# Performance work log

Measured on AMD Instinct MI355X. Metric: run time of the kernel, lower is better.

The kernel has to match this reference:

```python
import jax, jax.numpy as jnp
import numpy as np

B, L, D, H, NE, M, NP, C, F2 = 2, 1024, 768, 12, 42, 8, 1722, 97, 256


def setup_inputs() -> dict:
    key = jax.random.key(0)
    ks = jax.random.split(key, 12)
    s = 0.02
    sequence_output = jax.random.normal(ks[0], (B, L, D), jnp.float32)
    attention = jax.random.uniform(ks[1], (B, H, L, L), jnp.float32)
    mention_idx = jax.random.randint(ks[2], (B, NE, M), 0, L)
    mention_mask = jax.random.randint(ks[3], (B, NE, M), 0, 2).at[:, :, 0].set(1)
    hts = jax.random.randint(ks[4], (B, NP, 2), 0, NE)
    return dict(
        sequence_output=sequence_output, attention=attention,
        mention_idx=mention_idx, mention_mask=mention_mask, hts=hts,
        W_lin=jax.random.normal(ks[5], (D, 3)) * s, b_lin=jnp.zeros((3,)),
        W_seg=jax.random.normal(ks[6], (3, F2)) * s, b_seg=jnp.zeros((F2,)),
        W_head=jax.random.normal(ks[7], (D, F2)) * s, b_head=jnp.zeros((F2,)),
        W_tail=jax.random.normal(ks[8], (D, F2)) * s, b_tail=jnp.zeros((F2,)),
        W_bil=jax.random.normal(ks[9], (C, F2, F2)) * s, b_bil=jnp.zeros((C,)),
    )


def reference(sequence_output, attention, mention_idx, mention_mask, hts,
              W_lin, b_lin, W_seg, b_seg, W_head, b_head, W_tail, b_tail,
              W_bil, b_bil):
    b_, l_, d_ = sequence_output.shape
    h_ = attention.shape[1]
    ne, m_ = mention_idx.shape[1:]
    NEG = jnp.asarray(-1e30, sequence_output.dtype)
    msk = mention_mask.astype(sequence_output.dtype)  # [B,NE,M]

    bidx = jnp.arange(b_)[:, None, None]
    # --- get_hrt: per-entity mention gather + logsumexp pool / mean pool ---
    ment_emb = sequence_output[bidx, mention_idx]              # [B,NE,M,D]
    ent_emb = jax.nn.logsumexp(jnp.where(msk[..., None] > 0, ment_emb, NEG), axis=2)  # [B,NE,D]
    ment_att = attention[bidx, :, mention_idx]                 # [B,NE,M,H,L]
    ent_att = (ment_att * msk[..., None, None]).sum(2) / msk.sum(2)[..., None, None]  # [B,NE,H,L]

    b2 = jnp.arange(b_)[:, None]
    hs = ent_emb[b2, hts[..., 0]]                              # [B,NP,D]
    ts = ent_emb[b2, hts[..., 1]]

    # --- get_channel_map: all ne*ne pair attention-weighted context ---
    hi = jnp.repeat(jnp.arange(ne), ne)
    ti = jnp.tile(jnp.arange(ne), ne)
    h_att = ent_att[:, hi]                                     # [B,NE*NE,H,L]
    t_att = ent_att[:, ti]
    ht_att = jnp.einsum('bphl,bphl->bpl', h_att, t_att) / h_   # mean over heads
    ht_att = ht_att / (ht_att.sum(-1, keepdims=True) + 1e-5)
    rs = jnp.einsum('bld,bpl->bpd', sequence_output, ht_att)   # [B,NE*NE,D]
    feature_map = rs.reshape(b_, ne, ne, d_)

    # self.linear (D->3) then segmentation net (stand-in: 1x1 conv 3->F2 + relu)
    attn_input = feature_map @ W_lin + b_lin                   # [B,NE,NE,3]
    attn_map = jax.nn.relu(attn_input @ W_seg + b_seg)         # [B,NE,NE,F2]

    # --- get_ht: gather pair features ---
    h_t = attn_map[b2, hts[..., 0], hts[..., 1]]               # [B,NP,F2]
    hs = jnp.tanh(hs @ W_head + b_head + h_t)
    ts = jnp.tanh(ts @ W_tail + b_tail + h_t)
    logits = jnp.einsum('bpi,oij,bpj->bpo', hs, W_bil, ts) + b_bil
    return logits.reshape(-1, logits.shape[-1])               # [B*NP, C]
```

## Files before the change

kernel.cpp:

```cpp
#include <hip/hip_runtime.h>
#include <hip/hip_bf16.h>
#include <math.h>

constexpr int BB = 2;
constexpr int LL = 1024;
constexpr int DD = 768;
constexpr int HH = 12;
constexpr int NEz = 42;
constexpr int MM = 8;
constexpr int NPp = 1722;
constexpr int CC = 97;
constexpr int FF = 256;
constexpr int PAIRS = NEz * NEz;
constexpr int TOTAL = BB * NPp;
constexpr int MTv = 128;
constexpr int NTt = 28;
constexpr int PADR = 3584;
constexpr int NOGv = 36;
constexpr int NWGv = 1008;

typedef float f32x4 __attribute__((ext_vector_type(4)));
typedef short bf16x8 __attribute__((ext_vector_type(8)));
typedef unsigned int u32x2 __attribute__((ext_vector_type(2)));

__device__ inline short f2bs(float x) {
    __hip_bfloat16 b = __float2bfloat16(x);
    return *(short*)&b;
}
__device__ inline void gload16(const void* g, void* l) {
    __builtin_amdgcn_global_load_lds((const __attribute__((address_space(1))) unsigned int*)g,
                                     (__attribute__((address_space(3))) unsigned int*)l, 16, 0, 0);
}

__global__ void k_ent_emb(const float* __restrict__ seq, const int* __restrict__ midx,
                          const int* __restrict__ mmask, float* __restrict__ ent_emb) {
    int be = blockIdx.x;
    int b = be / NEz;
    int tid = threadIdx.x;
    int idx[MM], msk[MM];
#pragma unroll
    for (int m = 0; m < MM; ++m) {
        idx[m] = midx[be * MM + m];
        msk[m] = mmask[be * MM + m];
    }
    const float* sb = seq + (size_t)b * LL * DD;
    for (int d = tid; d < DD; d += 256) {
        float v[MM];
        float mx = -1e30f;
#pragma unroll
        for (int m = 0; m < MM; ++m) {
            v[m] = msk[m] ? sb[(size_t)idx[m] * DD + d] : -1e30f;
            mx = fmaxf(mx, v[m]);
        }
        float s = 0.f;
#pragma unroll
        for (int m = 0; m < MM; ++m) s += expf(v[m] - mx);
        ent_emb[(size_t)be * DD + d] = mx + logf(s);
    }
}

__global__ void k_ent_att(const float* __restrict__ att, const int* __restrict__ midx,
                          const int* __restrict__ mmask, float* __restrict__ ea) {
    int beh = blockIdx.x;
    int h = beh % HH;
    int be = beh / HH;
    int b = be / NEz;
    int tid = threadIdx.x;
    int idx[MM], msk[MM];
    float msum = 0.f;
#pragma unroll
    for (int m = 0; m < MM; ++m) {
        idx[m] = midx[be * MM + m];
        msk[m] = mmask[be * MM + m];
        msum += (float)msk[m];
    }
    float inv = 1.f / msum;
    const float* ab = att + ((size_t)b * HH + h) * LL * LL;
#pragma unroll
    for (int li = 0; li < 4; ++li) {
        int l = tid + li * 256;
        float acc = 0.f;
#pragma unroll
        for (int m = 0; m < MM; ++m)
            if (msk[m]) acc += ab[(size_t)idx[m] * LL + l];
        ea[(size_t)beh * LL + l] = acc * inv;
    }
}

__global__ void k_pairAB(const float* __restrict__ ea, const float* __restrict__ seq,
                         const float* __restrict__ Wl, float* __restrict__ szp) {
    int lcb = blockIdx.x;
    int b = blockIdx.y;
    int l0 = lcb * 8;
    int tid = threadIdx.x;
    int lane = tid & 63;
    int e1 = (tid >> 6) * 8 + (lane >> 3);
    int l = lane & 7;

    __shared__ float S[NEz][HH][9];
    __shared__ float sw[8][3];
    __shared__ float swp[24][17];

    for (int idx = tid; idx < NEz * HH * 8; idx += 384) {
        int e = idx / 96, rem = idx % 96;
        int h = rem / 8, ll = rem % 8;
        S[e][h][ll] = ea[((size_t)(b * NEz + e) * HH + h) * LL + l0 + ll];
    }
    {
        int cpair = tid % 24, s = tid / 24;
        if (s < 16) {
            int ll = cpair / 3, kk = cpair % 3;
            const float* sr = seq + ((size_t)b * LL + l0 + ll) * DD;
            float p = 0.f;
            for (int d = s * 48; d < s * 48 + 48; ++d) p += sr[d] * Wl[d * 3 + kk];
            swp[cpair][s] = p;
        }
    }
    __syncthreads();
    if (tid < 24) {
        float s = 0.f;
#pragma unroll
        for (int i = 0; i < 16; ++i) s += swp[tid][i];
        sw[tid / 3][tid % 3] = s;
    }
    __syncthreads();

    bool act = e1 < NEz;
    float e1r[HH];
#pragma unroll
    for (int h = 0; h < HH; ++h) e1r[h] = act ? S[e1][h][l] : 0.f;
    float sw0 = sw[l][0], sw1 = sw[l][1], sw2 = sw[l][2];

    for (int e2 = 0; e2 < NEz; ++e2) {
        float ht = 0.f;
#pragma unroll
        for (int h = 0; h < HH; ++h) ht += e1r[h] * S[e2][h][l];
        ht *= (1.0f / HH);
        float v0 = ht, v1 = ht * sw0, v2 = ht * sw1, v3 = ht * sw2;
#pragma unroll
        for (int off = 1; off < 8; off <<= 1) {
            v0 += __shfl_xor(v0, off);
            v1 += __shfl_xor(v1, off);
            v2 += __shfl_xor(v2, off);
            v3 += __shfl_xor(v3, off);
        }
        if (act && l == 0) {
            float4 o4 = make_float4(v0, v1, v2, v3);
            *(float4*)&szp[(((size_t)(b * PAIRS + e1 * NEz + e2)) * 128 + lcb) * 4] = o4;
        }
    }
}

__global__ void k_zz(const float* __restrict__ szp, const float* __restrict__ blin,
                     float* __restrict__ zz) {
    int idx = blockIdx.x * 256 + threadIdx.x;
    int bp = idx >> 3, s8 = idx & 7;
    if (bp >= BB * PAIRS) return;
    const float4* s = (const float4*)(szp + (size_t)bp * 512) + s8 * 16;
    float v0 = 0.f, v1 = 0.f, v2 = 0.f, v3 = 0.f;
#pragma unroll
    for (int i = 0; i < 16; ++i) {
        float4 a = s[i];
        v0 += a.x; v1 += a.y; v2 += a.z; v3 += a.w;
    }
#pragma unroll
    for (int off = 1; off < 8; off <<= 1) {
        v0 += __shfl_xor(v0, off);
        v1 += __shfl_xor(v1, off);
        v2 += __shfl_xor(v2, off);
        v3 += __shfl_xor(v3, off);
    }
    if (s8 == 0) {
        float inv = 1.f / (v0 + 1e-5f);
        float4 o4 = make_float4(v1 * inv + blin[0], v2 * inv + blin[1], v3 * inv + blin[2], 0.f);
        *(float4*)&zz[(size_t)bp * 4] = o4;
    }
}

__global__ void k_ew(const float* __restrict__ ent_emb, const float* __restrict__ Wh,
                     const float* __restrict__ bh, const float* __restrict__ Wt,
                     const float* __restrict__ bt, float* __restrict__ EWh,
                     float* __restrict__ EWt) {
    int be = blockIdx.x;
    int tid = threadIdx.x;
    __shared__ float e[DD];
    for (int d = tid; d < DD; d += 256) e[d] = ent_emb[(size_t)be * DD + d];
    __syncthreads();
    float ah = bh[tid], at = bt[tid];
    for (int d = 0; d < DD; ++d) {
        float ev = e[d];
        ah += ev * Wh[(size_t)d * FF + tid];
        at += ev * Wt[(size_t)d * FF + tid];
    }
    EWh[(size_t)be * FF + tid] = ah;
    EWt[(size_t)be * FF + tid] = at;
}

__global__ void k_wt(const float* __restrict__ Wb, char* __restrict__ Wf) {
    int o = blockIdx.x >> 2, kc = blockIdx.x & 3;
    int tid = threadIdx.x;
    __shared__ float t64[64][257];
    const float* src = Wb + (size_t)o * FF * FF + (size_t)(kc * 64) * FF;
#pragma unroll
    for (int i = 0; i < 64; ++i) {
        int flat = i * 256 + tid;
        t64[flat >> 8][flat & 255] = src[flat];
    }
    __syncthreads();
    char* dst = Wf + ((size_t)o * 4 + kc) * 32768;
#pragma unroll
    for (int i = 0; i < 8; ++i) {
        int u = i * 256 + tid;
        int c = u >> 3, k16 = u & 7;
        bf16x8 v;
#pragma unroll
        for (int j = 0; j < 8; ++j) v[j] = f2bs(t64[k16 * 8 + j][c]);
        *(bf16x8*)(dst + ((c * 128 + k16 * 16) ^ ((c & 7) << 4))) = v;
    }
}

__global__ void k_prep(const float* __restrict__ EWh, const float* __restrict__ EWt,
                       const float* __restrict__ zz, const float* __restrict__ Wseg,
                       const float* __restrict__ bseg, const int* __restrict__ hts,
                       char* __restrict__ HSf, unsigned short* __restrict__ TSt) {
    int tile = blockIdx.x >> 1, half = blockIdx.x & 1;
    int tid = threadIdx.x;
    int p0 = tile * MTv;

    __shared__ int offh[128];
    __shared__ float zr[128][3];
    __shared__ float wsg[4][128];
    __shared__ float Et[128][133];

    if (tid < 128) {
        int p = p0 + tid;
        if (p < TOTAL) {
            int b = p / NPp;
            int e1 = hts[p * 2], e2 = hts[p * 2 + 1];
            offh[tid] = (b * NEz + e1) * FF;
            float4 z4 = *(const float4*)(zz + (size_t)(b * PAIRS + e1 * NEz + e2) * 4);
            zr[tid][0] = z4.x; zr[tid][1] = z4.y; zr[tid][2] = z4.z;
        } else {
            offh[tid] = -1;
            zr[tid][0] = zr[tid][1] = zr[tid][2] = 0.f;
        }
        int c = half * 128 + tid;
        wsg[0][tid] = Wseg[c];
        wsg[1][tid] = Wseg[FF + c];
        wsg[2][tid] = Wseg[2 * FF + c];
        wsg[3][tid] = bseg[c];
    }
    {
        int r2 = tid >> 1, hc = tid & 1;
        int p = p0 + r2;
        int ot = -1;
        if (p < TOTAL) {
            int b = p / NPp;
            int e2 = hts[p * 2 + 1];
            ot = (b * NEz + e2) * FF;
        }
#pragma unroll
        for (int j = 0; j < 64; j += 4) {
            float4 v = make_float4(0.f, 0.f, 0.f, 0.f);
            if (ot >= 0) v = *(const float4*)(EWt + ot + half * 128 + hc * 64 + j);
            int cl = hc * 64 + j;
            Et[r2][cl] = v.x; Et[r2][cl + 1] = v.y; Et[r2][cl + 2] = v.z; Et[r2][cl + 3] = v.w;
        }
    }
    __syncthreads();

    char* dst = HSf + (size_t)tile * 65536;
#pragma unroll
    for (int i = 0; i < 8; ++i) {
        int u = i * 256 + tid;
        int r = u >> 4, k16 = u & 15;
        int oh = offh[r];
        bf16x8 v = {0, 0, 0, 0, 0, 0, 0, 0};
        if (oh >= 0) {
#pragma unroll
            for (int j = 0; j < 8; ++j) {
                int cl = k16 * 8 + j;
                float ht = fmaxf(zr[r][0] * wsg[0][cl] + zr[r][1] * wsg[1][cl] +
                                 zr[r][2] * wsg[2][cl] + wsg[3][cl], 0.f);
                v[j] = f2bs(tanhf(EWh[oh + half * 128 + cl] + ht));
            }
        }
        int byte = (r * 512 + half * 256 + k16 * 16) ^ ((r & 7) << 4);
        *(bf16x8*)(dst + byte) = v;
    }
    {
        int r = tid & 127, cg = tid >> 7;
        int p = p0 + r;
        bool act = p < TOTAL;
        for (int i2 = 0; i2 < 64; ++i2) {
            int cl = cg * 64 + i2;
            unsigned short v = 0;
            if (act) {
                float ht = fmaxf(zr[r][0] * wsg[0][cl] + zr[r][1] * wsg[1][cl] +
                                 zr[r][2] * wsg[2][cl] + wsg[3][cl], 0.f);
                v = (unsigned short)f2bs(tanhf(Et[r][cl] + ht));
            }
            TSt[(size_t)(half * 128 + cl) * PADR + p0 + r] = v;
        }
    }
}

#define STAGE(C, BUF) do { \
    int c_ = (C); \
    int o_ = og + NOGv * (c_ >> 2); \
    int kc_ = c_ & 3; \
    const char* Bs_ = Wf + ((size_t)(o_ * 4 + kc_)) * 32768; \
    _Pragma("unroll") \
    for (int i_ = 0; i_ < 4; ++i_) \
        gload16(Bs_ + (i_ * 512 + tid) * 16, Bb[BUF] + (i_ * 512 + tid) * 16); \
} while (0)

__launch_bounds__(512, 2)
__global__ void k_bil(const char* __restrict__ HSf, const unsigned short* __restrict__ TSt,
                      const char* __restrict__ Wf, const float* __restrict__ bbil,
                      float* __restrict__ out) {
    int f = blockIdx.x;
    int x = f & 7, sub = f >> 3;
    int q = x >> 1, h = x & 1;
    int og = q * 9 + sub / 14;
    int mt = h * 14 + sub % 14;
    int p0 = mt * MTv;
    int nO = (og < 25) ? 3 : 2;

    int tid = threadIdx.x;
    int lane = tid & 63, w = tid >> 6;
    int wr = w >> 2, wc = w & 3;
    int lr = lane & 15, lg = lane >> 4;

    __shared__ char A_l[65536];
    __shared__ char Bb[2][32768];
    __shared__ float red[MTv][4];

    u32x2 tsv[4][4];
#pragma unroll
    for (int mi = 0; mi < 4; ++mi)
#pragma unroll
        for (int ni = 0; ni < 4; ++ni)
            tsv[mi][ni] = *(const u32x2*)(TSt + (size_t)(wc * 64 + ni * 16 + lr) * PADR +
                                          p0 + wr * 64 + mi * 16 + lg * 4);

    {
        const char* As = HSf + (size_t)mt * 65536;
#pragma unroll
        for (int i = 0; i < 8; ++i)
            gload16(As + (i * 512 + tid) * 16, A_l + (i * 512 + tid) * 16);
    }
    STAGE(0, 0);
    STAGE(1, 1);

    f32x4 acc[4][4];
#pragma unroll
    for (int mi = 0; mi < 4; ++mi)
#pragma unroll
        for (int ni = 0; ni < 4; ++ni) acc[mi][ni] = (f32x4){0.f, 0.f, 0.f, 0.f};

    int T = 4 * nO;
    for (int t = 0; t < T; ++t) {
        int cur = t & 1;
        int kc = t & 3;
        __builtin_amdgcn_sched_barrier(0);
        asm volatile("s_waitcnt vmcnt(4)" ::: "memory");
        __builtin_amdgcn_sched_barrier(0);
        __builtin_amdgcn_s_barrier();
        __builtin_amdgcn_sched_barrier(0);

        const char* Bc = Bb[cur];
        int kA = kc * 128 + lg * 16;
        int kB = kA + 64;

        bf16x8 a0[4], b0[4];
#pragma unroll
        for (int mi = 0; mi < 4; ++mi) {
            int r = wr * 64 + mi * 16 + lr;
            a0[mi] = *(const bf16x8*)(A_l + ((r * 512 + kA) ^ ((r & 7) << 4)));
        }
#pragma unroll
        for (int ni = 0; ni < 4; ++ni) {
            int c = wc * 64 + ni * 16 + lr;
            b0[ni] = *(const bf16x8*)(Bc + ((c * 128 + lg * 16) ^ ((c & 7) << 4)));
        }
        __builtin_amdgcn_sched_barrier(0);
        asm volatile("s_waitcnt lgkmcnt(0)" ::: "memory");
        __builtin_amdgcn_sched_barrier(0);
        __builtin_amdgcn_s_setprio(1);
#pragma unroll
        for (int mi = 0; mi < 4; ++mi)
#pragma unroll
            for (int ni = 0; ni < 4; ++ni)
                acc[mi][ni] = __builtin_amdgcn_mfma_f32_16x16x32_bf16(a0[mi], b0[ni], acc[mi][ni], 0, 0, 0);
        __builtin_amdgcn_s_setprio(0);

        bf16x8 a1[4], b1[4];
#pragma unroll
        for (int mi = 0; mi < 4; ++mi) {
            int r = wr * 64 + mi * 16 + lr;
            a1[mi] = *(const bf16x8*)(A_l + ((r * 512 + kB) ^ ((r & 7) << 4)));
        }
#pragma unroll
        for (int ni = 0; ni < 4; ++ni) {
            int c = wc * 64 + ni * 16 + lr;
            b1[ni] = *(const bf16x8*)(Bc + ((c * 128 + 64 + lg * 16) ^ ((c & 7) << 4)));
        }
        __builtin_amdgcn_sched_barrier(0);
        asm volatile("s_waitcnt lgkmcnt(0)" ::: "memory");
        __builtin_amdgcn_sched_barrier(0);
        __builtin_amdgcn_s_barrier();
        __builtin_amdgcn_sched_barrier(0);

        int tt = (t + 2 < T) ? t + 2 : T - 1;
        STAGE(tt, cur);
        __builtin_amdgcn_sched_barrier(0);
        __builtin_amdgcn_s_setprio(1);
#pragma unroll
        for (int mi = 0; mi < 4; ++mi)
#pragma unroll
            for (int ni = 0; ni < 4; ++ni)
                acc[mi][ni] = __builtin_amdgcn_mfma_f32_16x16x32_bf16(a1[mi], b1[ni], acc[mi][ni], 0, 0, 0);
        __builtin_amdgcn_s_setprio(0);

        if ((t & 3) == 3) {
            int o = og + NOGv * (t >> 2);
#pragma unroll
            for (int mi = 0; mi < 4; ++mi) {
                float s0 = 0.f, s1 = 0.f, s2 = 0.f, s3 = 0.f;
#pragma unroll
                for (int ni = 0; ni < 4; ++ni) {
                    unsigned lo = tsv[mi][ni][0], hi = tsv[mi][ni][1];
                    s0 += acc[mi][ni][0] * __uint_as_float(lo << 16);
                    s1 += acc[mi][ni][1] * __uint_as_float(lo & 0xFFFF0000u);
                    s2 += acc[mi][ni][2] * __uint_as_float(hi << 16);
                    s3 += acc[mi][ni][3] * __uint_as_float(hi & 0xFFFF0000u);
                    acc[mi][ni] = (f32x4){0.f, 0.f, 0.f, 0.f};
                }
#pragma unroll
                for (int off = 1; off < 16; off <<= 1) {
                    s0 += __shfl_xor(s0, off);
                    s1 += __shfl_xor(s1, off);
                    s2 += __shfl_xor(s2, off);
                    s3 += __shfl_xor(s3, off);
                }
                if (lr == 0) {
                    int rb = wr * 64 + mi * 16 + lg * 4;
                    red[rb + 0][wc] = s0;
                    red[rb + 1][wc] = s1;
                    red[rb + 2][wc] = s2;
                    red[rb + 3][wc] = s3;
                }
            }
            __builtin_amdgcn_sched_barrier(0);
            asm volatile("s_waitcnt lgkmcnt(0)" ::: "memory");
            __builtin_amdgcn_sched_barrier(0);
            __builtin_amdgcn_s_barrier();
            __builtin_amdgcn_sched_barrier(0);
            if (tid < MTv) {
                int p = p0 + tid;
                if (p < TOTAL)
                    out[(size_t)p * CC + o] =
                        red[tid][0] + red[tid][1] + red[tid][2] + red[tid][3] + bbil[o];
            }
        }
    }
}
#undef STAGE

extern "C" void kernel_launch(void* const* d_in, const int* in_sizes, int n_in,
                              void* d_out, int out_size, void* d_ws, size_t ws_size,
                              hipStream_t stream) {
    const float* seq   = (const float*)d_in[0];
    const float* att   = (const float*)d_in[1];
    const int*   midx  = (const int*)d_in[2];
    const int*   mmask = (const int*)d_in[3];
    const int*   hts   = (const int*)d_in[4];
    const float* Wlin  = (const float*)d_in[5];
    const float* blin  = (const float*)d_in[6];
    const float* Wseg  = (const float*)d_in[7];
    const float* bseg  = (const float*)d_in[8];
    const float* Whead = (const float*)d_in[9];
    const float* bhead = (const float*)d_in[10];
    const float* Wtail = (const float*)d_in[11];
    const float* btail = (const float*)d_in[12];
    const float* Wbil  = (const float*)d_in[13];
    const float* bbil  = (const float*)d_in[14];
    float* out = (float*)d_out;

    float* ws = (float*)d_ws;
    float* ent_emb = ws;
    float* ea      = ent_emb + BB * NEz * DD;
    float* szp     = ea + (size_t)BB * NEz * HH * LL;
    float* zz      = szp + (size_t)BB * PAIRS * 128 * 4;
    float* EWh     = zz + (size_t)BB * PAIRS * 4;
    float* EWt     = EWh + BB * NEz * FF;
    char* Wf       = (char*)(EWt + BB * NEz * FF);
    char* HSf      = Wf + (size_t)CC * 4 * 32768;
    unsigned short* TSt = (unsigned short*)(HSf + (size_t)NTt * 65536);

    k_ent_emb<<<BB * NEz, 256, 0, stream>>>(seq, midx, mmask, ent_emb);
    k_ent_att<<<BB * NEz * HH, 256, 0, stream>>>(att, midx, mmask, ea);
    k_pairAB<<<dim3(128, BB), 384, 0, stream>>>(ea, seq, Wlin, szp);
    k_zz<<<(BB * PAIRS * 8 + 255) / 256, 256, 0, stream>>>(szp, blin, zz);
    k_ew<<<BB * NEz, 256, 0, stream>>>(ent_emb, Whead, bhead, Wtail, btail, EWh, EWt);
    k_wt<<<CC * 4, 256, 0, stream>>>(Wbil, Wf);
    k_prep<<<NTt * 2, 256, 0, stream>>>(EWh, EWt, zz, Wseg, bseg, hts, HSf, TSt);
    k_bil<<<NWGv, 512, 0, stream>>>(HSf, TSt, Wf, bbil, out);
}
```

Measured before the change: 199.0 us.

## Split bilinear K across workgroups with 256-row tiles and atomic accumulation

The bilinear kernel now uses 256-pair M tiles and splits the 256-wide reduction into two halves handled by different workgroups. Partial logits are combined with atomicAdd into an output zeroed by a memset, and the bias is added only by the first half. The head/tail projection kernel is split four ways along D, writing partial sums that the prep kernel adds up. The prep kernel is rebuilt to emit per-K-chunk swizzled A tiles and vectorized transposed tail stores. The aim is more reuse of each staged W_bil block and more parallelism in the small kernels, at the cost of atomics, an extra memset, and higher register pressure from the doubled accumulator tile.

```diff
diff --git a/kernel.cpp b/kernel.cpp
--- a/kernel.cpp
+++ b/kernel.cpp
@@ -13,11 +13,12 @@
 constexpr int FF = 256;
 constexpr int PAIRS = NEz * NEz;
 constexpr int TOTAL = BB * NPp;
-constexpr int MTv = 128;
-constexpr int NTt = 28;
+constexpr int MTv = 256;
+constexpr int NTt = 14;
 constexpr int PADR = 3584;
 constexpr int NOGv = 36;
 constexpr int NWGv = 1008;
+constexpr int EWSZ = BB * NEz * FF;
 
 typedef float f32x4 __attribute__((ext_vector_type(4)));
 typedef short bf16x8 __attribute__((ext_vector_type(8)));
@@ -179,21 +180,25 @@
 
 __global__ void k_ew(const float* __restrict__ ent_emb, const float* __restrict__ Wh,
                      const float* __restrict__ bh, const float* __restrict__ Wt,
-                     const float* __restrict__ bt, float* __restrict__ EWh,
-                     float* __restrict__ EWt) {
+                     const float* __restrict__ bt, float* __restrict__ EWph,
+                     float* __restrict__ EWpt) {
     int be = blockIdx.x;
-    int tid = threadIdx.x;
-    __shared__ float e[DD];
-    for (int d = tid; d < DD; d += 256) e[d] = ent_emb[(size_t)be * DD + d];
+    int dc = blockIdx.y;
+    int tid = threadIdx.x;
+    __shared__ float e[192];
+    if (tid < 192) e[tid] = ent_emb[(size_t)be * DD + dc * 192 + tid];
     __syncthreads();
-    float ah = bh[tid], at = bt[tid];
-    for (int d = 0; d < DD; ++d) {
+    float ah = (dc == 0) ? bh[tid] : 0.f;
+    float at = (dc == 0) ? bt[tid] : 0.f;
+    const float* Whb = Wh + (size_t)dc * 192 * FF;
+    const float* Wtb = Wt + (size_t)dc * 192 * FF;
+    for (int d = 0; d < 192; ++d) {
         float ev = e[d];
-        ah += ev * Wh[(size_t)d * FF + tid];
-        at += ev * Wt[(size_t)d * FF + tid];
-    }
-    EWh[(size_t)be * FF + tid] = ah;
-    EWt[(size_t)be * FF + tid] = at;
+        ah += ev * Whb[(size_t)d * FF + tid];
+        at += ev * Wtb[(size_t)d * FF + tid];
+    }
+    EWph[(size_t)dc * EWSZ + be * FF + tid] = ah;
+    EWpt[(size_t)dc * EWSZ + be * FF + tid] = at;
 }
 
 __global__ void k_wt(const float* __restrict__ Wb, char* __restrict__ Wf) {
@@ -219,96 +224,96 @@
     }
 }
 
-__global__ void k_prep(const float* __restrict__ EWh, const float* __restrict__ EWt,
+__global__ void k_prep(const float* __restrict__ EWph, const float* __restrict__ EWpt,
                        const float* __restrict__ zz, const float* __restrict__ Wseg,
                        const float* __restrict__ bseg, const int* __restrict__ hts,
                        char* __restrict__ HSf, unsigned short* __restrict__ TSt) {
-    int tile = blockIdx.x >> 1, half = blockIdx.x & 1;
-    int tid = threadIdx.x;
-    int p0 = tile * MTv;
-
-    __shared__ int offh[128];
-    __shared__ float zr[128][3];
-    __shared__ float wsg[4][128];
-    __shared__ float Et[128][133];
-
-    if (tid < 128) {
+    int mt = blockIdx.x >> 2, kc = blockIdx.x & 3;
+    int tid = threadIdx.x;
+    int p0 = mt * MTv;
+
+    __shared__ int offh[256], offt[256];
+    __shared__ float zr[256][3];
+    __shared__ float wsg[4][64];
+
+    {
         int p = p0 + tid;
         if (p < TOTAL) {
             int b = p / NPp;
             int e1 = hts[p * 2], e2 = hts[p * 2 + 1];
             offh[tid] = (b * NEz + e1) * FF;
+            offt[tid] = (b * NEz + e2) * FF;
             float4 z4 = *(const float4*)(zz + (size_t)(b * PAIRS + e1 * NEz + e2) * 4);
             zr[tid][0] = z4.x; zr[tid][1] = z4.y; zr[tid][2] = z4.z;
         } else {
-            offh[tid] = -1;
+            offh[tid] = -1; offt[tid] = -1;
             zr[tid][0] = zr[tid][1] = zr[tid][2] = 0.f;
         }
-        int c = half * 128 + tid;
-        wsg[0][tid] = Wseg[c];
-        wsg[1][tid] = Wseg[FF + c];
-        wsg[2][tid] = Wseg[2 * FF + c];
-        wsg[3][tid] = bseg[c];
-    }
-    {
-        int r2 = tid >> 1, hc = tid & 1;
-        int p = p0 + r2;
-        int ot = -1;
-        if (p < TOTAL) {
-            int b = p / NPp;
-            int e2 = hts[p * 2 + 1];
-            ot = (b * NEz + e2) * FF;
-        }
-#pragma unroll
-        for (int j = 0; j < 64; j += 4) {
-            float4 v = make_float4(0.f, 0.f, 0.f, 0.f);
-            if (ot >= 0) v = *(const float4*)(EWt + ot + half * 128 + hc * 64 + j);
-            int cl = hc * 64 + j;
-            Et[r2][cl] = v.x; Et[r2][cl + 1] = v.y; Et[r2][cl + 2] = v.z; Et[r2][cl + 3] = v.w;
+        if (tid < 64) {
+            int c = kc * 64 + tid;
+            wsg[0][tid] = Wseg[c];
+            wsg[1][tid] = Wseg[FF + c];
+            wsg[2][tid] = Wseg[2 * FF + c];
+            wsg[3][tid] = bseg[c];
         }
     }
     __syncthreads();
 
-    char* dst = HSf + (size_t)tile * 65536;
-#pragma unroll
-    for (int i = 0; i < 8; ++i) {
-        int u = i * 256 + tid;
-        int r = u >> 4, k16 = u & 15;
+    char* dst = HSf + (size_t)(mt * 4 + kc) * 32768;
+#pragma unroll
+    for (int it = 0; it < 8; ++it) {
+        int slot = it * 256 + tid;
+        int r = slot >> 3;
+        int kin = (slot & 7) * 16;
+        int kb = kin ^ ((r & 7) << 4);
+        int cl0 = kb >> 1;
         int oh = offh[r];
         bf16x8 v = {0, 0, 0, 0, 0, 0, 0, 0};
         if (oh >= 0) {
+            float z0 = zr[r][0], z1 = zr[r][1], z2 = zr[r][2];
+            int gc = oh + kc * 64 + cl0;
 #pragma unroll
             for (int j = 0; j < 8; ++j) {
-                int cl = k16 * 8 + j;
-                float ht = fmaxf(zr[r][0] * wsg[0][cl] + zr[r][1] * wsg[1][cl] +
-                                 zr[r][2] * wsg[2][cl] + wsg[3][cl], 0.f);
-                v[j] = f2bs(tanhf(EWh[oh + half * 128 + cl] + ht));
+                int cl = cl0 + j;
+                float ew = EWph[gc + j] + EWph[EWSZ + gc + j] +
+                           EWph[2 * EWSZ + gc + j] + EWph[3 * EWSZ + gc + j];
+                float ht = fmaxf(z0 * wsg[0][cl] + z1 * wsg[1][cl] +
+                                 z2 * wsg[2][cl] + wsg[3][cl], 0.f);
+                v[j] = f2bs(tanhf(ew + ht));
             }
         }
-        int byte = (r * 512 + half * 256 + k16 * 16) ^ ((r & 7) << 4);
-        *(bf16x8*)(dst + byte) = v;
+        *(bf16x8*)(dst + r * 128 + kin) = v;
     }
     {
-        int r = tid & 127, cg = tid >> 7;
-        int p = p0 + r;
-        bool act = p < TOTAL;
-        for (int i2 = 0; i2 < 64; ++i2) {
-            int cl = cg * 64 + i2;
-            unsigned short v = 0;
-            if (act) {
-                float ht = fmaxf(zr[r][0] * wsg[0][cl] + zr[r][1] * wsg[1][cl] +
-                                 zr[r][2] * wsg[2][cl] + wsg[3][cl], 0.f);
-                v = (unsigned short)f2bs(tanhf(Et[r][cl] + ht));
+        int cl = tid >> 2, rgg = tid & 3;
+        int c = kc * 64 + cl;
+        float w0 = wsg[0][cl], w1 = wsg[1][cl], w2 = wsg[2][cl], w3 = wsg[3][cl];
+#pragma unroll
+        for (int v8 = 0; v8 < 8; ++v8) {
+            int rbase = rgg * 64 + v8 * 8;
+            bf16x8 w;
+#pragma unroll
+            for (int j = 0; j < 8; ++j) {
+                int r = rbase + j;
+                int ot = offt[r];
+                short vv = 0;
+                if (ot >= 0) {
+                    float ew = EWpt[ot + c] + EWpt[EWSZ + ot + c] +
+                               EWpt[2 * EWSZ + ot + c] + EWpt[3 * EWSZ + ot + c];
+                    float ht = fmaxf(zr[r][0] * w0 + zr[r][1] * w1 + zr[r][2] * w2 + w3, 0.f);
+                    vv = f2bs(tanhf(ew + ht));
+                }
+                w[j] = vv;
             }
-            TSt[(size_t)(half * 128 + cl) * PADR + p0 + r] = v;
+            *(bf16x8*)(TSt + (size_t)c * PADR + p0 + rbase) = w;
         }
     }
 }
 
 #define STAGE(C, BUF) do { \
     int c_ = (C); \
-    int o_ = og + NOGv * (c_ >> 2); \
-    int kc_ = c_ & 3; \
+    int o_ = og + NOGv * (c_ >> 1); \
+    int kc_ = kr2 + (c_ & 1); \
     const char* Bs_ = Wf + ((size_t)(o_ * 4 + kc_)) * 32768; \
     _Pragma("unroll") \
     for (int i_ = 0; i_ < 4; ++i_) \
@@ -320,10 +325,11 @@
                       const char* __restrict__ Wf, const float* __restrict__ bbil,
                       float* __restrict__ out) {
     int f = blockIdx.x;
-    int x = f & 7, sub = f >> 3;
-    int q = x >> 1, h = x & 1;
-    int og = q * 9 + sub / 14;
-    int mt = h * 14 + sub % 14;
+    int xcd = f & 7, sub = f >> 3;
+    int q = xcd >> 1, kr = xcd & 1;
+    int og = q + 4 * (sub / 14);
+    int mt = sub % 14;
+    int kr2 = kr * 2;
     int p0 = mt * MTv;
     int nO = (og < 25) ? 3 : 2;
 
@@ -336,48 +342,49 @@
     __shared__ char Bb[2][32768];
     __shared__ float red[MTv][4];
 
-    u32x2 tsv[4][4];
-#pragma unroll
-    for (int mi = 0; mi < 4; ++mi)
+    u32x2 tsv[8][4];
+#pragma unroll
+    for (int mi = 0; mi < 8; ++mi)
 #pragma unroll
         for (int ni = 0; ni < 4; ++ni)
             tsv[mi][ni] = *(const u32x2*)(TSt + (size_t)(wc * 64 + ni * 16 + lr) * PADR +
-                                          p0 + wr * 64 + mi * 16 + lg * 4);
+                                          p0 + wr * 128 + mi * 16 + lg * 4);
+    __builtin_amdgcn_sched_barrier(0);
 
     {
-        const char* As = HSf + (size_t)mt * 65536;
+        const char* As = HSf + (size_t)(mt * 4 + kr2) * 32768;
 #pragma unroll
         for (int i = 0; i < 8; ++i)
             gload16(As + (i * 512 + tid) * 16, A_l + (i * 512 + tid) * 16);
     }
+    __builtin_amdgcn_sched_barrier(0);
     STAGE(0, 0);
+    __builtin_amdgcn_sched_barrier(0);
     STAGE(1, 1);
 
-    f32x4 acc[4][4];
-#pragma unroll
-    for (int mi = 0; mi < 4; ++mi)
+    f32x4 acc[8][4];
+#pragma unroll
+    for (int mi = 0; mi < 8; ++mi)
 #pragma unroll
         for (int ni = 0; ni < 4; ++ni) acc[mi][ni] = (f32x4){0.f, 0.f, 0.f, 0.f};
 
-    int T = 4 * nO;
+    int T = 2 * nO;
     for (int t = 0; t < T; ++t) {
         int cur = t & 1;
-        int kc = t & 3;
         __builtin_amdgcn_sched_barrier(0);
         asm volatile("s_waitcnt vmcnt(4)" ::: "memory");
         __builtin_amdgcn_sched_barrier(0);
         __builtin_amdgcn_s_barrier();
         __builtin_amdgcn_sched_barrier(0);
 
+        const char* Ac = A_l + cur * 32768;
         const char* Bc = Bb[cur];
-        int kA = kc * 128 + lg * 16;
-        int kB = kA + 64;
-
-        bf16x8 a0[4], b0[4];
-#pragma unroll
-        for (int mi = 0; mi < 4; ++mi) {
-            int r = wr * 64 + mi * 16 + lr;
-            a0[mi] = *(const bf16x8*)(A_l + ((r * 512 + kA) ^ ((r & 7) << 4)));
+
+        bf16x8 a0[8], b0[4];
+#pragma unroll
+        for (int mi = 0; mi < 8; ++mi) {
+            int r = wr * 128 + mi * 16 + lr;
+            a0[mi] = *(const bf16x8*)(Ac + ((r * 128 + lg * 16) ^ ((r & 7) << 4)));
         }
 #pragma unroll
         for (int ni = 0; ni < 4; ++ni) {
@@ -389,17 +396,17 @@
         __builtin_amdgcn_sched_barrier(0);
         __builtin_amdgcn_s_setprio(1);
 #pragma unroll
-        for (int mi = 0; mi < 4; ++mi)
+        for (int mi = 0; mi < 8; ++mi)
 #pragma unroll
             for (int ni = 0; ni < 4; ++ni)
                 acc[mi][ni] = __builtin_amdgcn_mfma_f32_16x16x32_bf16(a0[mi], b0[ni], acc[mi][ni], 0, 0, 0);
         __builtin_amdgcn_s_setprio(0);
 
-        bf16x8 a1[4], b1[4];
-#pragma unroll
-        for (int mi = 0; mi < 4; ++mi) {
-            int r = wr * 64 + mi * 16 + lr;
-            a1[mi] = *(const bf16x8*)(A_l + ((r * 512 + kB) ^ ((r & 7) << 4)));
+        bf16x8 a1[8], b1[4];
+#pragma unroll
+        for (int mi = 0; mi < 8; ++mi) {
+            int r = wr * 128 + mi * 16 + lr;
+            a1[mi] = *(const bf16x8*)(Ac + ((r * 128 + 64 + lg * 16) ^ ((r & 7) << 4)));
         }
 #pragma unroll
         for (int ni = 0; ni < 4; ++ni) {
@@ -417,16 +424,16 @@
         __builtin_amdgcn_sched_barrier(0);
         __builtin_amdgcn_s_setprio(1);
 #pragma unroll
-        for (int mi = 0; mi < 4; ++mi)
+        for (int mi = 0; mi < 8; ++mi)
 #pragma unroll
             for (int ni = 0; ni < 4; ++ni)
                 acc[mi][ni] = __builtin_amdgcn_mfma_f32_16x16x32_bf16(a1[mi], b1[ni], acc[mi][ni], 0, 0, 0);
         __builtin_amdgcn_s_setprio(0);
 
-        if ((t & 3) == 3) {
-            int o = og + NOGv * (t >> 2);
-#pragma unroll
-            for (int mi = 0; mi < 4; ++mi) {
+        if (t & 1) {
+            int o = og + NOGv * (t >> 1);
+#pragma unroll
+            for (int mi = 0; mi < 8; ++mi) {
                 float s0 = 0.f, s1 = 0.f, s2 = 0.f, s3 = 0.f;
 #pragma unroll
                 for (int ni = 0; ni < 4; ++ni) {
@@ -445,7 +452,7 @@
                     s3 += __shfl_xor(s3, off);
                 }
                 if (lr == 0) {
-                    int rb = wr * 64 + mi * 16 + lg * 4;
+                    int rb = wr * 128 + mi * 16 + lg * 4;
                     red[rb + 0][wc] = s0;
                     red[rb + 1][wc] = s1;
                     red[rb + 2][wc] = s2;
@@ -459,9 +466,11 @@
             __builtin_amdgcn_sched_barrier(0);
             if (tid < MTv) {
                 int p = p0 + tid;
-                if (p < TOTAL)
-                    out[(size_t)p * CC + o] =
-                        red[tid][0] + red[tid][1] + red[tid][2] + red[tid][3] + bbil[o];
+                if (p < TOTAL) {
+                    float v = red[tid][0] + red[tid][1] + red[tid][2] + red[tid][3] +
+                              (kr == 0 ? bbil[o] : 0.f);
+                    atomicAdd(out + (size_t)p * CC + o, v);
+                }
             }
         }
     }
@@ -493,18 +502,19 @@
     float* ea      = ent_emb + BB * NEz * DD;
     float* szp     = ea + (size_t)BB * NEz * HH * LL;
     float* zz      = szp + (size_t)BB * PAIRS * 128 * 4;
-    float* EWh     = zz + (size_t)BB * PAIRS * 4;
-    float* EWt     = EWh + BB * NEz * FF;
-    char* Wf       = (char*)(EWt + BB * NEz * FF);
+    float* EWph    = zz + (size_t)BB * PAIRS * 4;
+    float* EWpt    = EWph + 4 * EWSZ;
+    char* Wf       = (char*)(EWpt + 4 * EWSZ);
     char* HSf      = Wf + (size_t)CC * 4 * 32768;
-    unsigned short* TSt = (unsigned short*)(HSf + (size_t)NTt * 65536);
-
+    unsigned short* TSt = (unsigned short*)(HSf + (size_t)NTt * 4 * 32768);
+
+    hipMemsetAsync(out, 0, (size_t)out_size * sizeof(float), stream);
     k_ent_emb<<<BB * NEz, 256, 0, stream>>>(seq, midx, mmask, ent_emb);
     k_ent_att<<<BB * NEz * HH, 256, 0, stream>>>(att, midx, mmask, ea);
     k_pairAB<<<dim3(128, BB), 384, 0, stream>>>(ea, seq, Wlin, szp);
     k_zz<<<(BB * PAIRS * 8 + 255) / 256, 256, 0, stream>>>(szp, blin, zz);
-    k_ew<<<BB * NEz, 256, 0, stream>>>(ent_emb, Whead, bhead, Wtail, btail, EWh, EWt);
+    k_ew<<<dim3(BB * NEz, 4), 256, 0, stream>>>(ent_emb, Whead, bhead, Wtail, btail, EWph, EWpt);
     k_wt<<<CC * 4, 256, 0, stream>>>(Wbil, Wf);
-    k_prep<<<NTt * 2, 256, 0, stream>>>(EWh, EWt, zz, Wseg, bseg, hts, HSf, TSt);
+    k_prep<<<NTt * 4, 256, 0, stream>>>(EWph, EWpt, zz, Wseg, bseg, hts, HSf, TSt);
     k_bil<<<NWGv, 512, 0, stream>>>(HSf, TSt, Wf, bbil, out);
 }
```

After: 491.3 us. 147% more time.
